# Kernel tuning notes

Hardware: AMD Instinct MI355X
Metric: run time of the kernel (lower is better)

## Reference

```python
import jax, jax.numpy as jnp
import numpy as np

POS_NUM = 60
TWO_PI = 2.0 * np.pi


def setup_inputs() -> dict:
    key = jax.random.key(0)
    k1, k2 = jax.random.split(key)
    B = 262144
    # [r1, r3, r4, r5, thc]; positive link lengths / angle in a realistic range
    pred_tensor = jax.random.uniform(k1, (B, 5), minval=0.1, maxval=2.0, dtype=jnp.float32)
    target_tensor = jax.random.normal(k2, (B, 2 * POS_NUM), dtype=jnp.float32)
    return {"pred_tensor": pred_tensor, "target_tensor": target_tensor}


def _compute_pos(pred, th2_min, th2_max, n):
    """Vectorized version of PosLoss.compute_pos.
    pred: [B,9] = [r1,r2,r3,r4,th1,r5,alpha,x0,y0]; th2_min/th2_max: [B].
    Returns interleaved coupler positions [B, 2n] = [x0,y0,x1,y1,...]."""
    dt = pred.dtype
    step = (th2_max - th2_min) / (n - 1)                     # [B]
    th2 = th2_min[:, None] + step[:, None] * jnp.arange(n, dtype=dt)  # [B,n]
    r1, r2, r3, r4 = pred[:, 0:1], pred[:, 1:2], pred[:, 2:3], pred[:, 3:4]
    th1, r5, al = pred[:, 4:5], pred[:, 5:6], pred[:, 6:7]
    x0, y0 = pred[:, 7:8], pred[:, 8:9]
    k1 = r1**2 + r2**2 + r3**2 - r4**2 - 2.0 * r1 * r2 * jnp.cos(th2 - th1)
    k2 = 2.0 * r1 * r3 * jnp.cos(th1) - 2.0 * r2 * r3 * jnp.cos(th2)
    k3 = 2.0 * r1 * r3 * jnp.sin(th1) - 2.0 * r2 * r3 * jnp.sin(th2)
    a = k1 + k2
    b = -2.0 * k3
    c = k1 - k2
    disc = b * b - 4.0 * a * c
    bad = disc < 0                                            # == isnan(sqrt(disc))
    D = jnp.sqrt(jnp.where(bad, 0.0, disc))
    th3 = 2.0 * jnp.arctan((-b + D) / (2.0 * a))
    p1x = jnp.where(bad, 0.0, r2 * jnp.cos(th2) + r5 * jnp.cos(al + th3) + x0)
    p1y = jnp.where(bad, 0.0, r2 * jnp.sin(th2) + r5 * jnp.sin(al + th3) + y0)
    return jnp.stack([p1x, p1y], axis=-1).reshape(pred.shape[0], 2 * n)


def reference(pred_tensor, target_tensor):
    n = POS_NUM
    dt = pred_tensor.dtype
    B = pred_tensor.shape[0]
    zeros = jnp.zeros((B,), dt)
    ones = jnp.ones((B,), dt)
    # pred9 = [r1, r2=1, r3, r4, th1=0, r5, alpha=thc, x0=0, y0=0]
    pred9 = jnp.stack([pred_tensor[:, 0], ones, pred_tensor[:, 1], pred_tensor[:, 2],
                       zeros, pred_tensor[:, 3], pred_tensor[:, 4], zeros, zeros], axis=1)
    L = pred9[:, :4]
    valid = 2.0 * jnp.max(L, axis=1) < jnp.sum(L, axis=1)
    c1 = (L[:, 0] + L[:, 1] - (L[:, 2] + L[:, 3])) > 0
    c2 = (jnp.abs(L[:, 0] - L[:, 1]) - jnp.abs(L[:, 2] - L[:, 3])) >= 0
    up = valid & c1 & c2
    low = valid & (~c1) & (~c2)
    bo = valid & c1 & (~c2)
    no = valid & (~c1) & c2
    denom = 2.0 * L[:, 0] * L[:, 1]
    arg_sum = (L[:, 0] ** 2 + L[:, 1] ** 2 - (L[:, 2] + L[:, 3]) ** 2) / denom
    arg_diff = (L[:, 0] ** 2 + L[:, 1] ** 2 - (L[:, 2] - L[:, 3]) ** 2) / denom
    acos_sum = jnp.arccos(jnp.where(up | bo, arg_sum, 0.0))
    acos_diff = jnp.arccos(jnp.where(low | bo, arg_diff, 0.0))
    th2_min = jnp.where(up, -acos_sum, jnp.where(low | bo, acos_diff, 0.0))
    th2_max = jnp.where(up | bo, acos_sum, jnp.where(low, TWO_PI - acos_diff, TWO_PI))
    # Sanitize rows that never contribute (invalid) so no NaN/Inf leaks in.
    safe_row = jnp.asarray([2.0, 1.0, 2.0, 2.0, 0.0, 1.0, 0.0, 0.0, 0.0], dt)
    pred_eff = jnp.where(valid[:, None], pred9, safe_row)
    th2_min = jnp.where(valid, th2_min, 0.0)
    th2_max = jnp.where(valid, th2_max, TWO_PI)
    pos = _compute_pos(pred_eff, th2_min, th2_max, n)         # [B, 2n]
    sq = (pos - target_tensor) ** 2

    def msum(m, x):
        return jnp.sum(jnp.where(m[:, None], x, 0.0))

    invalid_loss = msum(~valid, target_tensor ** 2)           # pos == 0 for invalid rows
    up_loss = msum(up, sq)
    low_loss = msum(low, sq)
    bo_loss = msum(bo, sq)
    no_loss = msum(no, sq)
    Nf = jnp.asarray(B, dt)
    return (invalid_loss / Nf, up_loss / Nf, low_loss / Nf, bo_loss / Nf, no_loss / Nf)
```

## Files before the change

### kernel.cpp

```cpp
#include <hip/hip_runtime.h>
#include <math.h>

#define CHUNK 32
#define NPOS 60
#define TWO_PI_F 6.283185307179586f
#define INV_TWO_PI_F 0.15915494309189535f
#define PI_F 3.14159265358979f

__device__ __forceinline__ float bcastf(float v, int l) {
    return __builtin_bit_cast(float, __builtin_amdgcn_readlane(__builtin_bit_cast(int, v), l));
}

__device__ __forceinline__ float acos_poly(float x) {
    const float ax = fabsf(x);
    const float s = __builtin_amdgcn_sqrtf(fmaxf(0.0f, 1.0f - ax));
    float p = fmaf(ax, -0.0187293f, 0.0742610f);
    p = fmaf(ax, p, -0.2121144f);
    p = fmaf(ax, p, 1.5707288f);
    const float r = s * p;
    return (x < 0.0f) ? (PI_F - r) : r;
}

__device__ __forceinline__ void hw_sincos_rev(float rev, float* s, float* c) {
    const float f = __builtin_amdgcn_fractf(rev);
    *s = __builtin_amdgcn_sinf(f);
    *c = __builtin_amdgcn_cosf(f);
}

__device__ __forceinline__ void row_acc(
    int rr, float txj, float tyj, float flane, bool inpos,
    float th2min_rev, float stp_rev, float ca5, float sa5,
    float P, float Q, float R, float S, float Bb, int cat,
    float& a0, float& a1, float& a2, float& a3, float& a4)
{
    const int catr    = __builtin_amdgcn_readlane(cat, rr);
    const float rev0  = bcastf(th2min_rev, rr);
    const float stp_r = bcastf(stp_rev, rr);
    const float ca5_r = bcastf(ca5, rr);
    const float sa5_r = bcastf(sa5, rr);
    const float P_r   = bcastf(P, rr);
    const float Q_r   = bcastf(Q, rr);
    const float R_r   = bcastf(R, rr);
    const float S_r   = bcastf(S, rr);
    const float Bb_r  = bcastf(Bb, rr);

    const float rev = fmaf(stp_r, flane, rev0);
    float sth, cth;
    hw_sincos_rev(rev, &sth, &cth);
    const float a  = fmaf(-Q_r, cth, P_r);
    const float cc = fmaf(-S_r, cth, R_r);
    const float b  = Bb_r * sth;
    const float disc = fmaf(b, b, -4.0f * (a * cc));
    const bool bad = disc < 0.0f;
    const float D = __builtin_amdgcn_sqrtf(fmaxf(disc, 0.0f));
    const float w = D - b;
    const float s = a + a;
    const float s2 = s * s, w2 = w * w;
    const float rden = __builtin_amdgcn_rcpf(s2 + w2);
    const float c3 = (s2 - w2) * rden;
    const float sw = s * w;
    const float s3 = (sw + sw) * rden;
    float px = fmaf(ca5_r, c3, fmaf(-sa5_r, s3, cth));
    float py = fmaf(sa5_r, c3, fmaf(ca5_r, s3, sth));
    px = bad ? 0.0f : px;
    py = bad ? 0.0f : py;
    const float dx = px - txj, dy = py - tyj;
    float ch = fmaf(dx, dx, dy * dy);
    ch = inpos ? ch : 0.0f;
    float c0 = fmaf(txj, txj, tyj * tyj);
    c0 = inpos ? c0 : 0.0f;
    a0 += (catr == 0) ? c0 : 0.0f;
    a1 += (catr == 1) ? ch : 0.0f;
    a2 += (catr == 2) ? ch : 0.0f;
    a3 += (catr == 3) ? ch : 0.0f;
    a4 += (catr == 4) ? ch : 0.0f;
}

__device__ __forceinline__ float2 ldt(const float* __restrict__ target,
                                      int base, int rr, int lpos) {
    return *reinterpret_cast<const float2*>(
        target + (size_t)(base + rr) * (size_t)(2 * NPOS) + 2 * lpos);
}

#define LOADB(Pfx, r0)                                                                 \
    do {                                                                               \
        float2 _v;                                                                     \
        _v = ldt(target, base, (r0) + 0, lpos); Pfx##x0 = _v.x; Pfx##y0 = _v.y;        \
        _v = ldt(target, base, (r0) + 1, lpos); Pfx##x1 = _v.x; Pfx##y1 = _v.y;        \
        _v = ldt(target, base, (r0) + 2, lpos); Pfx##x2 = _v.x; Pfx##y2 = _v.y;        \
        _v = ldt(target, base, (r0) + 3, lpos); Pfx##x3 = _v.x; Pfx##y3 = _v.y;        \
        _v = ldt(target, base, (r0) + 4, lpos); Pfx##x4 = _v.x; Pfx##y4 = _v.y;        \
        _v = ldt(target, base, (r0) + 5, lpos); Pfx##x5 = _v.x; Pfx##y5 = _v.y;        \
        _v = ldt(target, base, (r0) + 6, lpos); Pfx##x6 = _v.x; Pfx##y6 = _v.y;        \
        _v = ldt(target, base, (r0) + 7, lpos); Pfx##x7 = _v.x; Pfx##y7 = _v.y;        \
    } while (0)

#define ROWA(Pfx, rr, sx, sy)                                                          \
    row_acc((rr), Pfx##sx, Pfx##sy, flane, inpos, th2min_rev, stp_rev, ca5, sa5,       \
            Pc, Qc, Rc, Sc, Bb, cat, a0, a1, a2, a3, a4)

#define COMPUTEB(Pfx, r0)                                                              \
    do {                                                                               \
        ROWA(Pfx, (r0) + 0, x0, y0);                                                   \
        ROWA(Pfx, (r0) + 1, x1, y1);                                                   \
        ROWA(Pfx, (r0) + 2, x2, y2);                                                   \
        ROWA(Pfx, (r0) + 3, x3, y3);                                                   \
        ROWA(Pfx, (r0) + 4, x4, y4);                                                   \
        ROWA(Pfx, (r0) + 5, x5, y5);                                                   \
        ROWA(Pfx, (r0) + 6, x6, y6);                                                   \
        ROWA(Pfx, (r0) + 7, x7, y7);                                                   \
    } while (0)

__global__ __launch_bounds__(256, 6) void posloss_main(
    const float* __restrict__ pred, const float* __restrict__ target,
    float* __restrict__ partials, int B, int nchunks)
{
    const int tid  = threadIdx.x;
    const int lane = tid & 63;
    const int wv   = tid >> 6;
    const int wid  = (blockIdx.x * blockDim.x + tid) >> 6;
    const bool inpos = lane < NPOS;
    const int lpos = inpos ? lane : (NPOS - 1);
    const float flane = (float)lane;

    float a0 = 0.f, a1 = 0.f, a2 = 0.f, a3 = 0.f, a4 = 0.f;

    if (wid < nchunks) {
        const int base = wid * CHUNK;
        const int rmax = (B - base) < CHUNK ? (B - base) : CHUNK;

        const int prow = base + (lane & 31);
        float r1 = 2.f, r3 = 2.f, r4 = 2.f, r5 = 1.f, al = 0.f;
        if (prow < B) {
            const float* pp = pred + (size_t)prow * 5;
            r1 = pp[0]; r3 = pp[1]; r4 = pp[2]; r5 = pp[3]; al = pp[4];
        }

        const float sumL = ((r1 + 1.0f) + r3) + r4;
        const float maxL = fmaxf(fmaxf(r1, 1.0f), fmaxf(r3, r4));
        const bool valid = (2.0f * maxL) < sumL;
        const bool c1 = ((r1 + 1.0f) - (r3 + r4)) > 0.0f;
        const bool c2 = (fabsf(r1 - 1.0f) - fabsf(r3 - r4)) >= 0.0f;
        const bool up = valid && c1 && c2;
        const bool lo = valid && (!c1) && (!c2);
        const bool bo = valid && c1 && (!c2);
        const float rdenom = __builtin_amdgcn_rcpf(2.0f * r1);
        const float s34 = r3 + r4, d34 = r3 - r4;
        const float r1sq1 = fmaf(r1, r1, 1.0f);
        float argS = (r1sq1 - s34 * s34) * rdenom;
        float argD = (r1sq1 - d34 * d34) * rdenom;
        argS = (up || bo) ? argS : 0.0f;
        argD = (lo || bo) ? argD : 0.0f;
        argS = fminf(1.0f, fmaxf(-1.0f, argS));
        argD = fminf(1.0f, fmaxf(-1.0f, argD));
        const float acS = acos_poly(argS);
        const float acD = acos_poly(argD);
        float th2min = up ? (-acS) : ((lo || bo) ? acD : 0.0f);
        float th2max = (up || bo) ? acS : (lo ? (TWO_PI_F - acD) : TWO_PI_F);
        if (!valid) { th2min = 0.0f; th2max = TWO_PI_F; }
        const float stp_rev    = (th2max - th2min) * (INV_TWO_PI_F / 59.0f);
        const float th2min_rev = th2min * INV_TWO_PI_F;
        const int cat = (!valid) ? 0 : (up ? 1 : (lo ? 2 : (bo ? 3 : 4)));
        float sal, cal;
        hw_sincos_rev(al * INV_TWO_PI_F, &sal, &cal);
        const float ca5 = r5 * cal, sa5 = r5 * sal;
        const float K1c = fmaf(r3, r3, r1sq1) - r4 * r4;
        const float K1m = 2.0f * r1;
        const float A2  = (2.0f * r1) * r3;
        const float B2  = 2.0f * r3;
        const float Pc = K1c + A2;
        const float Qc = K1m + B2;
        const float Rc = K1c - A2;
        const float Sc = K1m - B2;
        const float Bb = 2.0f * B2;

        if (rmax == CHUNK) {
            float Ax0,Ay0,Ax1,Ay1,Ax2,Ay2,Ax3,Ay3,Ax4,Ay4,Ax5,Ay5,Ax6,Ay6,Ax7,Ay7;
            float Bx0,By0,Bx1,By1,Bx2,By2,Bx3,By3,Bx4,By4,Bx5,By5,Bx6,By6,Bx7,By7;
            LOADB(A, 0);
            LOADB(B, 8);
            COMPUTEB(A, 0);
            LOADB(A, 16);
            COMPUTEB(B, 8);
            LOADB(B, 24);
            COMPUTEB(A, 16);
            COMPUTEB(B, 24);
        } else {
            for (int rr = 0; rr < rmax; ++rr) {
                const float2 tv = ldt(target, base, rr, lpos);
                row_acc(rr, tv.x, tv.y, flane, inpos, th2min_rev, stp_rev, ca5, sa5,
                        Pc, Qc, Rc, Sc, Bb, cat, a0, a1, a2, a3, a4);
            }
        }
    }

    for (int off = 32; off; off >>= 1) {
        a0 += __shfl_xor(a0, off);
        a1 += __shfl_xor(a1, off);
        a2 += __shfl_xor(a2, off);
        a3 += __shfl_xor(a3, off);
        a4 += __shfl_xor(a4, off);
    }
    __shared__ float red[4][5];
    if (lane == 0) {
        red[wv][0] = a0; red[wv][1] = a1; red[wv][2] = a2; red[wv][3] = a3; red[wv][4] = a4;
    }
    __syncthreads();
    if (tid < 5) {
        const float s = ((red[0][tid] + red[1][tid]) + red[2][tid]) + red[3][tid];
        partials[(size_t)tid * gridDim.x + blockIdx.x] = s;
    }
}

__global__ void posloss_reduce(const float* __restrict__ partials, float* __restrict__ out,
                               int nblocks, int B)
{
    const int w = threadIdx.x >> 6, lane = threadIdx.x & 63;
    if (w >= 5) return;
    double s0 = 0.0, s1 = 0.0, s2 = 0.0, s3 = 0.0;
    const float* p = partials + (size_t)w * nblocks;
    for (int k = lane; k + 192 < nblocks; k += 256) {
        s0 += (double)p[k];
        s1 += (double)p[k + 64];
        s2 += (double)p[k + 128];
        s3 += (double)p[k + 192];
    }
    double s = (s0 + s1) + (s2 + s3);
    for (int off = 32; off; off >>= 1) s += __shfl_down(s, off);
    if (lane == 0) out[w] = (float)(s / (double)B);
}

extern "C" void kernel_launch(void* const* d_in, const int* in_sizes, int n_in,
                              void* d_out, int out_size, void* d_ws, size_t ws_size,
                              hipStream_t stream) {
    (void)n_in; (void)out_size; (void)ws_size;
    const float* pred   = (const float*)d_in[0];
    const float* target = (const float*)d_in[1];
    float* out = (float*)d_out;
    float* partials = (float*)d_ws;
    const int B = in_sizes[0] / 5;
    const int nchunks = (B + CHUNK - 1) / CHUNK;
    const int nblocks = 2048;
    posloss_main<<<nblocks, 256, 0, stream>>>(pred, target, partials, B, nchunks);
    posloss_reduce<<<1, 320, 0, stream>>>(partials, out, nblocks, B);
}
```

Measured before the change: 39.52 us.

## Stream target rows into LDS via async global_load_lds with staged waitcnt

Each wave now handles 16 rows instead of 32, and blocks grow from 4 to 8 waves. All of a wave's target rows are issued up front as direct global-to-LDS loads, two rows per 1 KB segment. The per-row parameter setup then runs while those loads are in flight. Compute for each segment starts after an explicit vmcnt wait, so it overlaps with the loads still pending. This is meant to hide global load latency and cut VGPR pressure from register-staged targets. The cost is 64 KB of LDS per block, which can limit occupancy, plus clamped duplicate loads at the tail.

```diff
diff --git a/kernel.cpp b/kernel.cpp
--- a/kernel.cpp
+++ b/kernel.cpp
@@ -1,11 +1,16 @@
 #include <hip/hip_runtime.h>
 #include <math.h>
 
-#define CHUNK 32
 #define NPOS 60
+#define CHUNK 16
+#define NSEG 8
+#define SEGB 1024
+#define WPB 8
 #define TWO_PI_F 6.283185307179586f
 #define INV_TWO_PI_F 0.15915494309189535f
 #define PI_F 3.14159265358979f
+
+typedef __attribute__((ext_vector_type(2))) float f32x2;
 
 __device__ __forceinline__ float bcastf(float v, int l) {
     return __builtin_bit_cast(float, __builtin_amdgcn_readlane(__builtin_bit_cast(int, v), l));
@@ -28,12 +33,13 @@
 }
 
 __device__ __forceinline__ void row_acc(
-    int rr, float txj, float tyj, float flane, bool inpos,
+    int rr, int rmax, float txj, float tyj, float flane, bool inpos,
     float th2min_rev, float stp_rev, float ca5, float sa5,
     float P, float Q, float R, float S, float Bb, int cat,
     float& a0, float& a1, float& a2, float& a3, float& a4)
 {
-    const int catr    = __builtin_amdgcn_readlane(cat, rr);
+    int catr = __builtin_amdgcn_readlane(cat, rr);
+    catr = (rr < rmax) ? catr : -1;
     const float rev0  = bcastf(th2min_rev, rr);
     const float stp_r = bcastf(stp_rev, rr);
     const float ca5_r = bcastf(ca5, rr);
@@ -76,49 +82,31 @@
     a4 += (catr == 4) ? ch : 0.0f;
 }
 
-__device__ __forceinline__ float2 ldt(const float* __restrict__ target,
-                                      int base, int rr, int lpos) {
-    return *reinterpret_cast<const float2*>(
-        target + (size_t)(base + rr) * (size_t)(2 * NPOS) + 2 * lpos);
-}
-
-#define LOADB(Pfx, r0)                                                                 \
-    do {                                                                               \
-        float2 _v;                                                                     \
-        _v = ldt(target, base, (r0) + 0, lpos); Pfx##x0 = _v.x; Pfx##y0 = _v.y;        \
-        _v = ldt(target, base, (r0) + 1, lpos); Pfx##x1 = _v.x; Pfx##y1 = _v.y;        \
-        _v = ldt(target, base, (r0) + 2, lpos); Pfx##x2 = _v.x; Pfx##y2 = _v.y;        \
-        _v = ldt(target, base, (r0) + 3, lpos); Pfx##x3 = _v.x; Pfx##y3 = _v.y;        \
-        _v = ldt(target, base, (r0) + 4, lpos); Pfx##x4 = _v.x; Pfx##y4 = _v.y;        \
-        _v = ldt(target, base, (r0) + 5, lpos); Pfx##x5 = _v.x; Pfx##y5 = _v.y;        \
-        _v = ldt(target, base, (r0) + 6, lpos); Pfx##x6 = _v.x; Pfx##y6 = _v.y;        \
-        _v = ldt(target, base, (r0) + 7, lpos); Pfx##x7 = _v.x; Pfx##y7 = _v.y;        \
+#define ROWACC(rr, tx_, ty_)                                                    \
+    row_acc((rr), rmax, (tx_), (ty_), flane, inpos, th2min_rev, stp_rev,        \
+            ca5, sa5, Pc, Qc, Rc, Sc, Bb, cat, a0, a1, a2, a3, a4)
+
+#define SEG(k, N)                                                               \
+    do {                                                                        \
+        asm volatile("s_waitcnt vmcnt(" #N ")" ::: "memory");                   \
+        __builtin_amdgcn_sched_barrier(0);                                      \
+        const f32x2 t0 = *(const f32x2*)(myseg + (k) * SEGB + 8 * lpos);        \
+        const f32x2 t1 = *(const f32x2*)(myseg + (k) * SEGB + 480 + 8 * lpos);  \
+        ROWACC(2 * (k),     t0.x, t0.y);                                        \
+        ROWACC(2 * (k) + 1, t1.x, t1.y);                                        \
     } while (0)
 
-#define ROWA(Pfx, rr, sx, sy)                                                          \
-    row_acc((rr), Pfx##sx, Pfx##sy, flane, inpos, th2min_rev, stp_rev, ca5, sa5,       \
-            Pc, Qc, Rc, Sc, Bb, cat, a0, a1, a2, a3, a4)
-
-#define COMPUTEB(Pfx, r0)                                                              \
-    do {                                                                               \
-        ROWA(Pfx, (r0) + 0, x0, y0);                                                   \
-        ROWA(Pfx, (r0) + 1, x1, y1);                                                   \
-        ROWA(Pfx, (r0) + 2, x2, y2);                                                   \
-        ROWA(Pfx, (r0) + 3, x3, y3);                                                   \
-        ROWA(Pfx, (r0) + 4, x4, y4);                                                   \
-        ROWA(Pfx, (r0) + 5, x5, y5);                                                   \
-        ROWA(Pfx, (r0) + 6, x6, y6);                                                   \
-        ROWA(Pfx, (r0) + 7, x7, y7);                                                   \
-    } while (0)
-
-__global__ __launch_bounds__(256, 6) void posloss_main(
+__global__ __launch_bounds__(512, 2) void posloss_main(
     const float* __restrict__ pred, const float* __restrict__ target,
     float* __restrict__ partials, int B, int nchunks)
 {
+    __shared__ char smem[WPB * NSEG * SEGB];
+    __shared__ float red[WPB][5];
+
     const int tid  = threadIdx.x;
     const int lane = tid & 63;
     const int wv   = tid >> 6;
-    const int wid  = (blockIdx.x * blockDim.x + tid) >> 6;
+    const int wid  = blockIdx.x * WPB + wv;
     const bool inpos = lane < NPOS;
     const int lpos = inpos ? lane : (NPOS - 1);
     const float flane = (float)lane;
@@ -128,12 +116,20 @@
     if (wid < nchunks) {
         const int base = wid * CHUNK;
         const int rmax = (B - base) < CHUNK ? (B - base) : CHUNK;
-
-        const int prow = base + (lane & 31);
-        float r1 = 2.f, r3 = 2.f, r4 = 2.f, r5 = 1.f, al = 0.f;
-        if (prow < B) {
-            const float* pp = pred + (size_t)prow * 5;
-            r1 = pp[0]; r3 = pp[1]; r4 = pp[2]; r5 = pp[3]; al = pp[4];
+        char* myseg = smem + wv * (NSEG * SEGB);
+
+        int prow = base + (lane & 15);
+        prow = prow < B ? prow : (B - 1);
+        const float* pp = pred + (size_t)prow * 5;
+        const float r1 = pp[0], r3 = pp[1], r4 = pp[2], r5 = pp[3], al = pp[4];
+
+        #pragma unroll
+        for (int k = 0; k < NSEG; ++k) {
+            int rb = base + 2 * k;
+            rb = rb <= (B - 2) ? rb : (B - 2);
+            const char* gsrc = (const char*)target + (size_t)rb * 480 + (size_t)lpos * 16;
+            __builtin_amdgcn_global_load_lds((const float*)gsrc,
+                                             (float*)(myseg + k * SEGB), 16, 0, 0);
         }
 
         const float sumL = ((r1 + 1.0f) + r3) + r4;
@@ -174,24 +170,14 @@
         const float Sc = K1m - B2;
         const float Bb = 2.0f * B2;
 
-        if (rmax == CHUNK) {
-            float Ax0,Ay0,Ax1,Ay1,Ax2,Ay2,Ax3,Ay3,Ax4,Ay4,Ax5,Ay5,Ax6,Ay6,Ax7,Ay7;
-            float Bx0,By0,Bx1,By1,Bx2,By2,Bx3,By3,Bx4,By4,Bx5,By5,Bx6,By6,Bx7,By7;
-            LOADB(A, 0);
-            LOADB(B, 8);
-            COMPUTEB(A, 0);
-            LOADB(A, 16);
-            COMPUTEB(B, 8);
-            LOADB(B, 24);
-            COMPUTEB(A, 16);
-            COMPUTEB(B, 24);
-        } else {
-            for (int rr = 0; rr < rmax; ++rr) {
-                const float2 tv = ldt(target, base, rr, lpos);
-                row_acc(rr, tv.x, tv.y, flane, inpos, th2min_rev, stp_rev, ca5, sa5,
-                        Pc, Qc, Rc, Sc, Bb, cat, a0, a1, a2, a3, a4);
-            }
-        }
+        SEG(0, 7);
+        SEG(1, 6);
+        SEG(2, 5);
+        SEG(3, 4);
+        SEG(4, 3);
+        SEG(5, 2);
+        SEG(6, 1);
+        SEG(7, 0);
     }
 
     for (int off = 32; off; off >>= 1) {
@@ -201,13 +187,14 @@
         a3 += __shfl_xor(a3, off);
         a4 += __shfl_xor(a4, off);
     }
-    __shared__ float red[4][5];
     if (lane == 0) {
         red[wv][0] = a0; red[wv][1] = a1; red[wv][2] = a2; red[wv][3] = a3; red[wv][4] = a4;
     }
     __syncthreads();
     if (tid < 5) {
-        const float s = ((red[0][tid] + red[1][tid]) + red[2][tid]) + red[3][tid];
+        float s = 0.0f;
+        #pragma unroll
+        for (int w = 0; w < WPB; ++w) s += red[w][tid];
         partials[(size_t)tid * gridDim.x + blockIdx.x] = s;
     }
 }
@@ -240,7 +227,7 @@
     float* partials = (float*)d_ws;
     const int B = in_sizes[0] / 5;
     const int nchunks = (B + CHUNK - 1) / CHUNK;
-    const int nblocks = 2048;
-    posloss_main<<<nblocks, 256, 0, stream>>>(pred, target, partials, B, nchunks);
+    const int nblocks = (nchunks + WPB - 1) / WPB;
+    posloss_main<<<nblocks, 512, 0, stream>>>(pred, target, partials, B, nchunks);
     posloss_reduce<<<1, 320, 0, stream>>>(partials, out, nblocks, B);
 }
```

Measured after the change: 46.09 us. 1.17x slower.
